# Optimization experiments

Hardware: AMD Instinct MI355X
Metric: run time of the kernel (lower is better)

The kernel has to match this reference:

```python
import jax, jax.numpy as jnp
import numpy as np

N_EMBD = 768
N_HEAD = 12
HEAD_DIM = N_EMBD // N_HEAD
EPS = 1e-6


def setup_inputs() -> dict:
    key = jax.random.key(0)
    ks = jax.random.split(key, 8)
    B, T, C = 4, 2048, N_EMBD
    s = 0.02
    return {
        "x": jax.random.normal(ks[0], (B, T, C), jnp.float32),
        "ln1_w": jnp.ones((C,), jnp.float32),
        "ln1_b": jnp.zeros((C,), jnp.float32),
        "W_attn": jax.random.normal(ks[1], (C, 3 * C), jnp.float32) * s,
        "b_attn": jnp.zeros((3 * C,), jnp.float32),
        "W_attn_proj": jax.random.normal(ks[2], (C, C), jnp.float32) * s,
        "b_attn_proj": jnp.zeros((C,), jnp.float32),
        "ln2_w": jnp.ones((C,), jnp.float32),
        "ln2_b": jnp.zeros((C,), jnp.float32),
        "W_fc": jax.random.normal(ks[3], (C, 4 * C), jnp.float32) * s,
        "b_fc": jnp.zeros((4 * C,), jnp.float32),
        "W_mlp_proj": jax.random.normal(ks[4], (4 * C, C), jnp.float32) * s,
        "b_mlp_proj": jnp.zeros((C,), jnp.float32),
    }


def layer_norm(x, w, b):
    # Faithful to MyLayerNorm: (x - mean) / (std + eps), std with ddof=0
    mean = jnp.mean(x, axis=-1, keepdims=True)
    std = jnp.sqrt(jnp.mean((x - mean) ** 2, axis=-1, keepdims=True))
    return w * (x - mean) / (std + EPS) + b


def attention(h, W_attn, b_attn, W_proj, b_proj):
    B, T, C = h.shape
    qkv = h @ W_attn + b_attn                      # [B,T,3C]
    q, k, v = jnp.split(qkv, 3, axis=-1)
    # [B,T,C] -> [B,H,T,D]
    def to_heads(t):
        return t.reshape(B, T, N_HEAD, HEAD_DIM).transpose(0, 2, 1, 3)
    q, k, v = to_heads(q), to_heads(k), to_heads(v)
    att = jnp.einsum("bhtd,bhsd->bhts", q, k) * (1.0 / np.sqrt(HEAD_DIM))
    causal = jnp.tril(jnp.ones((T, T), bool))[None, None]
    att = jnp.where(causal, att, -jnp.inf)
    att = jax.nn.softmax(att, axis=-1)
    y = jnp.einsum("bhts,bhsd->bhtd", att, v)      # [B,H,T,D]
    y = y.transpose(0, 2, 1, 3).reshape(B, T, C)
    return y @ W_proj + b_proj


def mlp(h, W_fc, b_fc, W_proj, b_proj):
    h = jax.nn.gelu(h @ W_fc + b_fc, approximate=False)
    return h @ W_proj + b_proj


def reference(x, ln1_w, ln1_b, W_attn, b_attn, W_attn_proj, b_attn_proj,
              ln2_w, ln2_b, W_fc, b_fc, W_mlp_proj, b_mlp_proj):
    x = x + attention(layer_norm(x, ln1_w, ln1_b), W_attn, b_attn, W_attn_proj, b_attn_proj)
    x = x + mlp(layer_norm(x, ln2_w, ln2_b), W_fc, b_fc, W_mlp_proj, b_mlp_proj)
    return x
```

## Files before the change

kernel.cpp:

```cpp
#include <hip/hip_runtime.h>
#include <hip/hip_bf16.h>
#include <math.h>

#define N_EMBD 768
#define N_HEAD 12
#define HEAD_DIM 64
#define TOKENS 8192
#define SEQ 2048
#define BATCH 4
#define NQT (SEQ / 64)

typedef __attribute__((ext_vector_type(8))) short short8;
typedef __attribute__((ext_vector_type(4))) float f32x4;

__device__ __forceinline__ short f2bf(float f) {
    unsigned u = __builtin_bit_cast(unsigned, f);
    unsigned r = (u + 0x7fffu + ((u >> 16) & 1u)) >> 16;
    return (short)r;
}
__device__ __forceinline__ short f2bf_fast(float f) {
    unsigned u = __builtin_bit_cast(unsigned, f);
    return (short)((u + 0x8000u) >> 16);
}

__device__ __forceinline__ float gelu_fast(float x) {
    float z = 1.5957691216057308f * x * (1.0f + 0.044715f * x * x);
    return x / (1.0f + __expf(-z));
}

__device__ __forceinline__ void gld16(const void* g, void* l) {
    __builtin_amdgcn_global_load_lds(
        (const __attribute__((address_space(1))) unsigned int*)g,
        (__attribute__((address_space(3))) unsigned int*)l, 16, 0, 0);
}

__global__ __launch_bounds__(256) void wT_kernel(const float* __restrict__ W,
                                                 short* __restrict__ Wt,
                                                 int K, int N) {
    __shared__ float T[32][33];
    int k0 = blockIdx.y * 32, n0 = blockIdx.x * 32;
    int c = threadIdx.x & 31, r0 = threadIdx.x >> 5;
#pragma unroll
    for (int i = 0; i < 32; i += 8)
        T[r0 + i][c] = W[(size_t)(k0 + r0 + i) * N + n0 + c];
    __syncthreads();
#pragma unroll
    for (int i = 0; i < 32; i += 8)
        Wt[(size_t)(n0 + r0 + i) * K + k0 + c] = f2bf(T[c][r0 + i]);
}

__global__ __launch_bounds__(256) void ln_bf_kernel(const float* __restrict__ x,
                                                    const float* __restrict__ w,
                                                    const float* __restrict__ b,
                                                    short* __restrict__ out) {
    int row = blockIdx.x;
    const float* xr = x + (size_t)row * N_EMBD;
    short* yr = out + (size_t)row * N_EMBD;
    __shared__ float red[256];
    int tid = threadIdx.x;
    float v0 = xr[tid], v1 = xr[tid + 256], v2 = xr[tid + 512];
    red[tid] = v0 + v1 + v2; __syncthreads();
    for (int off = 128; off > 0; off >>= 1) {
        if (tid < off) red[tid] += red[tid + off];
        __syncthreads();
    }
    float mean = red[0] * (1.f / 768.f);
    __syncthreads();
    float d0 = v0 - mean, d1 = v1 - mean, d2 = v2 - mean;
    red[tid] = d0 * d0 + d1 * d1 + d2 * d2; __syncthreads();
    for (int off = 128; off > 0; off >>= 1) {
        if (tid < off) red[tid] += red[tid + off];
        __syncthreads();
    }
    float inv = 1.f / (sqrtf(red[0] * (1.f / 768.f)) + 1e-6f);
    yr[tid]       = f2bf(w[tid]       * d0 * inv + b[tid]);
    yr[tid + 256] = f2bf(w[tid + 256] * d1 * inv + b[tid + 256]);
    yr[tid + 512] = f2bf(w[tid + 512] * d2 * inv + b[tid + 512]);
}

template <int ACT, int RES, int OUTBF>
__global__ __launch_bounds__(256) void gemm_mfma(
        const short* __restrict__ A,
        const short* __restrict__ Bt,
        const float* __restrict__ bias,
        const float* __restrict__ res,
        void* __restrict__ outp,
        int M, int N, int K) {
    __shared__ short As[8192];
    __shared__ short Bs[8192];
    int tid = threadIdx.x;
    int wave = tid >> 6, lane = tid & 63;
    int quad = lane >> 4, l15 = lane & 15;
    int m0 = blockIdx.x * 128, n0 = blockIdx.y * 128;
    int wm = wave >> 1, wn = wave & 1;
    int sr = lane >> 2, sc = (lane & 3) * 8;

    f32x4 acc[4][4];
#pragma unroll
    for (int i = 0; i < 4; ++i)
#pragma unroll
        for (int j = 0; j < 4; ++j) acc[i][j] = (f32x4){0.f, 0.f, 0.f, 0.f};

    const short* ag = A + (size_t)(m0 + wave * 32 + sr) * K + sc;
    const short* bg = Bt + (size_t)(n0 + wave * 32 + sr) * K + sc;
    int woff = wave * 1024;

    gld16(ag, &As[woff]);
    gld16(ag + (size_t)16 * K, &As[woff + 512]);
    gld16(bg, &Bs[woff]);
    gld16(bg + (size_t)16 * K, &Bs[woff + 512]);

    int nk = K >> 5;
    for (int it = 0; it < nk; ++it) {
        int cb = (it & 1) * 4096;
        __syncthreads();
        if (it + 1 < nk) {
            int nb = ((it + 1) & 1) * 4096 + woff;
            int kn = (it + 1) << 5;
            gld16(ag + kn, &As[nb]);
            gld16(ag + kn + (size_t)16 * K, &As[nb + 512]);
            gld16(bg + kn, &Bs[nb]);
            gld16(bg + kn + (size_t)16 * K, &Bs[nb + 512]);
        }
        short8 af[4], bfr[4];
#pragma unroll
        for (int mt = 0; mt < 4; ++mt)
            af[mt] = *(const short8*)&As[cb + (wm * 64 + mt * 16 + l15) * 32 + quad * 8];
#pragma unroll
        for (int nt = 0; nt < 4; ++nt)
            bfr[nt] = *(const short8*)&Bs[cb + (wn * 64 + nt * 16 + l15) * 32 + quad * 8];
#pragma unroll
        for (int mt = 0; mt < 4; ++mt)
#pragma unroll
            for (int nt = 0; nt < 4; ++nt)
                acc[mt][nt] = __builtin_amdgcn_mfma_f32_16x16x32_bf16(
                    af[mt], bfr[nt], acc[mt][nt], 0, 0, 0);
    }

#pragma unroll
    for (int mt = 0; mt < 4; ++mt) {
        int row0 = m0 + wm * 64 + mt * 16 + quad * 4;
#pragma unroll
        for (int nt = 0; nt < 4; ++nt) {
            int col = n0 + wn * 64 + nt * 16 + l15;
            float bi = bias[col];
#pragma unroll
            for (int r = 0; r < 4; ++r) {
                float v = acc[mt][nt][r] + bi;
                if (ACT == 1) v = gelu_fast(v);
                if (RES) v += res[(size_t)(row0 + r) * N + col];
                if (OUTBF) ((short*)outp)[(size_t)(row0 + r) * N + col] = f2bf(v);
                else       ((float*)outp)[(size_t)(row0 + r) * N + col] = v;
            }
        }
    }
}

template <int ACT, int RES, int OUTBF>
__global__ __launch_bounds__(256) void gemm_mfma_n64(
        const short* __restrict__ A,
        const short* __restrict__ Bt,
        const float* __restrict__ bias,
        const float* __restrict__ res,
        void* __restrict__ outp,
        int M, int N, int K) {
    __shared__ short As[8192];
    __shared__ short Bs[4096];
    int tid = threadIdx.x;
    int wave = tid >> 6, lane = tid & 63;
    int quad = lane >> 4, l15 = lane & 15;
    int m0 = blockIdx.x * 128, n0 = blockIdx.y * 64;
    int wm = wave >> 1, wn = wave & 1;
    int sr = lane >> 2, sc = (lane & 3) * 8;

    f32x4 acc[4][2];
#pragma unroll
    for (int i = 0; i < 4; ++i)
#pragma unroll
        for (int j = 0; j < 2; ++j) acc[i][j] = (f32x4){0.f, 0.f, 0.f, 0.f};

    const short* gptr[3];
    int loff[3];
    bool isa[3];
#pragma unroll
    for (int j = 0; j < 3; ++j) {
        int c = wave * 3 + j;
        if (c < 8) {
            gptr[j] = A + (size_t)(m0 + c * 16 + sr) * K + sc;
            loff[j] = c * 512; isa[j] = true;
        } else {
            gptr[j] = Bt + (size_t)(n0 + (c - 8) * 16 + sr) * K + sc;
            loff[j] = (c - 8) * 512; isa[j] = false;
        }
    }

#pragma unroll
    for (int j = 0; j < 3; ++j)
        gld16(gptr[j], isa[j] ? &As[loff[j]] : &Bs[loff[j]]);

    int nk = K >> 5;
    for (int it = 0; it < nk; ++it) {
        int cba = (it & 1) * 4096, cbb = (it & 1) * 2048;
        __syncthreads();
        if (it + 1 < nk) {
            int nba = ((it + 1) & 1) * 4096, nbb = ((it + 1) & 1) * 2048;
            int kn = (it + 1) << 5;
#pragma unroll
            for (int j = 0; j < 3; ++j)
                gld16(gptr[j] + kn, isa[j] ? &As[nba + loff[j]] : &Bs[nbb + loff[j]]);
        }
        short8 af[4], bfr[2];
#pragma unroll
        for (int mt = 0; mt < 4; ++mt)
            af[mt] = *(const short8*)&As[cba + (wm * 64 + mt * 16 + l15) * 32 + quad * 8];
#pragma unroll
        for (int nt = 0; nt < 2; ++nt)
            bfr[nt] = *(const short8*)&Bs[cbb + (wn * 32 + nt * 16 + l15) * 32 + quad * 8];
#pragma unroll
        for (int mt = 0; mt < 4; ++mt)
#pragma unroll
            for (int nt = 0; nt < 2; ++nt)
                acc[mt][nt] = __builtin_amdgcn_mfma_f32_16x16x32_bf16(
                    af[mt], bfr[nt], acc[mt][nt], 0, 0, 0);
    }

#pragma unroll
    for (int mt = 0; mt < 4; ++mt) {
        int row0 = m0 + wm * 64 + mt * 16 + quad * 4;
#pragma unroll
        for (int nt = 0; nt < 2; ++nt) {
            int col = n0 + wn * 32 + nt * 16 + l15;
            float bi = bias[col];
#pragma unroll
            for (int r = 0; r < 4; ++r) {
                float v = acc[mt][nt][r] + bi;
                if (ACT == 1) v = gelu_fast(v);
                if (RES) v += res[(size_t)(row0 + r) * N + col];
                if (OUTBF) ((short*)outp)[(size_t)(row0 + r) * N + col] = f2bf(v);
                else       ((float*)outp)[(size_t)(row0 + r) * N + col] = v;
            }
        }
    }
}

__global__ __launch_bounds__(256) void vT_kernel(const short* __restrict__ qkv,
                                                 short* __restrict__ Vt) {
    __shared__ short Ts[64][65];
    int t0 = blockIdx.x * 64;
    int bh = blockIdx.y;
    int h = bh % N_HEAD, b = bh / N_HEAD;
    int tid = threadIdx.x;
    int r = tid >> 3, c8 = (tid & 7) * 8;
    const short* src = qkv + ((size_t)(b * SEQ + t0)) * 2304 + 1536 + h * 64;
#pragma unroll
    for (int p = 0; p < 2; ++p) {
        int rr = r + p * 32;
        short8 v = *(const short8*)(src + (size_t)rr * 2304 + c8);
#pragma unroll
        for (int j = 0; j < 8; ++j) Ts[rr][c8 + j] = v[j];
    }
    __syncthreads();
    int d = tid >> 2, s0 = (tid & 3) * 16;
    short* dst = Vt + ((size_t)bh * 64 + d) * SEQ + t0;
#pragma unroll
    for (int p = 0; p < 2; ++p) {
        int sb = s0 + p * 8;
        short8 v;
#pragma unroll
        for (int j = 0; j < 8; ++j) v[j] = Ts[sb + j][d];
        *(short8*)(dst + sb) = v;
    }
}

__device__ __forceinline__ void attn_tile(
        const short* __restrict__ qkv, const short* __restrict__ Vt,
        short* __restrict__ y, int bh, int qt,
        short* Qs, short* Ks, short* Vs, short* Ps) {
    int tid = threadIdx.x;
    int wave = tid >> 6, lane = tid & 63;
    int quad = lane >> 4, l15 = lane & 15;
    int h = bh % N_HEAD, b = bh / N_HEAD;
    size_t bT = (size_t)b * SEQ;
    int q0 = qt * 64;
    int sr = lane >> 2, sc = (lane & 3) * 8;

    const short ONE_BF = (short)0x3F80;
    short8 ones;
#pragma unroll
    for (int j = 0; j < 8; ++j) ones[j] = ONE_BF;

    __syncthreads();
#pragma unroll
    for (int j = 0; j < 2; ++j) {
        int c = wave * 2 + j;
        int sub = c >> 2, r0 = (c & 3) * 16;
        const short* g = qkv + (bT + q0 + r0 + sr) * 2304 + h * 64 + sub * 32 + sc;
        gld16(g, &Qs[sub * 2048 + r0 * 32]);
    }
    __syncthreads();
    short8 qf[2];
    qf[0] = *(const short8*)&Qs[(wave * 16 + l15) * 32 + quad * 8];
    qf[1] = *(const short8*)&Qs[2048 + (wave * 16 + l15) * 32 + quad * 8];

    f32x4 o[4];
#pragma unroll
    for (int nt = 0; nt < 4; ++nt) o[nt] = (f32x4){0.f, 0.f, 0.f, 0.f};
    f32x4 lacc = (f32x4){0.f, 0.f, 0.f, 0.f};

    for (int kt = 0; kt <= qt; ++kt) {
        int k0 = kt * 64;
        __syncthreads();
#pragma unroll
        for (int j = 0; j < 4; ++j) {
            int c = wave * 4 + j;
            if (c < 8) {
                int sub = c >> 2, r0 = (c & 3) * 16;
                const short* g = qkv + (bT + k0 + r0 + sr) * 2304 + 768 + h * 64 + sub * 32 + sc;
                gld16(g, &Ks[sub * 2048 + r0 * 32]);
            } else {
                int cv = c - 8;
                int sub = cv >> 2, r0 = (cv & 3) * 16;
                const short* g = Vt + ((size_t)bh * 64 + r0 + sr) * SEQ + k0 + sub * 32 + sc;
                gld16(g, &Vs[sub * 2048 + r0 * 32]);
            }
        }
        __syncthreads();

        f32x4 sacc[4];
#pragma unroll
        for (int nt = 0; nt < 4; ++nt) sacc[nt] = (f32x4){0.f, 0.f, 0.f, 0.f};
#pragma unroll
        for (int nt = 0; nt < 4; ++nt)
#pragma unroll
            for (int ks = 0; ks < 2; ++ks) {
                short8 kf = *(const short8*)&Ks[ks * 2048 + (nt * 16 + l15) * 32 + quad * 8];
                sacc[nt] = __builtin_amdgcn_mfma_f32_16x16x32_bf16(qf[ks], kf, sacc[nt], 0, 0, 0);
            }

        bool diag = (kt == qt);
#pragma unroll
        for (int nt = 0; nt < 4; ++nt) {
            int scol = nt * 16 + l15;
            int base = (scol >> 5) * 2048 + (scol & 31);
#pragma unroll
            for (int r = 0; r < 4; ++r) {
                float s = sacc[nt][r] * 0.125f - 4.0f;
                if (diag && (scol > wave * 16 + quad * 4 + r)) s = -1e30f;
                Ps[base + (wave * 16 + quad * 4 + r) * 32] = f2bf_fast(__expf(s));
            }
        }

        short8 pf0 = *(const short8*)&Ps[(wave * 16 + l15) * 32 + quad * 8];
        short8 pf1 = *(const short8*)&Ps[2048 + (wave * 16 + l15) * 32 + quad * 8];
        lacc = __builtin_amdgcn_mfma_f32_16x16x32_bf16(pf0, ones, lacc, 0, 0, 0);
        lacc = __builtin_amdgcn_mfma_f32_16x16x32_bf16(pf1, ones, lacc, 0, 0, 0);
#pragma unroll
        for (int nt = 0; nt < 4; ++nt) {
            short8 vf0 = *(const short8*)&Vs[(nt * 16 + l15) * 32 + quad * 8];
            short8 vf1 = *(const short8*)&Vs[2048 + (nt * 16 + l15) * 32 + quad * 8];
            o[nt] = __builtin_amdgcn_mfma_f32_16x16x32_bf16(pf0, vf0, o[nt], 0, 0, 0);
            o[nt] = __builtin_amdgcn_mfma_f32_16x16x32_bf16(pf1, vf1, o[nt], 0, 0, 0);
        }
    }

    float inv[4];
#pragma unroll
    for (int r = 0; r < 4; ++r) inv[r] = 1.f / lacc[r];
#pragma unroll
    for (int nt = 0; nt < 4; ++nt)
#pragma unroll
        for (int r = 0; r < 4; ++r)
            y[(bT + q0 + wave * 16 + quad * 4 + r) * N_EMBD + h * 64 + nt * 16 + l15] =
                f2bf(o[nt][r] * inv[r]);
}

__global__ __launch_bounds__(256) void attn_mfma(
        const short* __restrict__ qkv, const short* __restrict__ Vt,
        short* __restrict__ y) {
    __shared__ short Qs[4096], Ks[4096], Vs[4096], Ps[4096];
    int bh = blockIdx.x;
    int pair = blockIdx.y;
    attn_tile(qkv, Vt, y, bh, pair, Qs, Ks, Vs, Ps);
    attn_tile(qkv, Vt, y, bh, NQT - 1 - pair, Qs, Ks, Vs, Ps);
}

extern "C" void kernel_launch(void* const* d_in, const int* in_sizes, int n_in,
                              void* d_out, int out_size, void* d_ws, size_t ws_size,
                              hipStream_t stream) {
    const float* x         = (const float*)d_in[0];
    const float* ln1_w     = (const float*)d_in[1];
    const float* ln1_b     = (const float*)d_in[2];
    const float* W_attn    = (const float*)d_in[3];
    const float* b_attn    = (const float*)d_in[4];
    const float* W_attn_pr = (const float*)d_in[5];
    const float* b_attn_pr = (const float*)d_in[6];
    const float* ln2_w     = (const float*)d_in[7];
    const float* ln2_b     = (const float*)d_in[8];
    const float* W_fc      = (const float*)d_in[9];
    const float* b_fc      = (const float*)d_in[10];
    const float* W_mlp_pr  = (const float*)d_in[11];
    const float* b_mlp_pr  = (const float*)d_in[12];
    float* out = (float*)d_out;

    const int M = TOKENS, C = N_EMBD;
    char* ws = (char*)d_ws;
    size_t region0 = (size_t)M * 3072 * 2;
    short* qkv_bf = (short*)ws;
    short* fc_bf  = (short*)ws;
    size_t off = region0;
    short* VtB   = (short*)(ws + off); off += (size_t)48 * 64 * SEQ * 2;
    short* yb    = (short*)(ws + off); off += (size_t)M * C * 2;
    short* lnb   = (short*)(ws + off); off += (size_t)M * C * 2;
    float* x1    = (float*)(ws + off); off += (size_t)M * C * 4;
    short* WaT   = (short*)(ws + off); off += (size_t)2304 * 768 * 2;
    short* WpT   = (short*)(ws + off); off += (size_t)768 * 768 * 2;
    short* WfT   = (short*)(ws + off); off += (size_t)3072 * 768 * 2;
    short* WmT   = (short*)(ws + off); off += (size_t)768 * 3072 * 2;

    wT_kernel<<<dim3(2304 / 32, 768 / 32), 256, 0, stream>>>(W_attn, WaT, 768, 2304);
    wT_kernel<<<dim3(768 / 32, 768 / 32), 256, 0, stream>>>(W_attn_pr, WpT, 768, 768);
    wT_kernel<<<dim3(3072 / 32, 768 / 32), 256, 0, stream>>>(W_fc, WfT, 768, 3072);
    wT_kernel<<<dim3(768 / 32, 3072 / 32), 256, 0, stream>>>(W_mlp_pr, WmT, 3072, 768);

    ln_bf_kernel<<<M, 256, 0, stream>>>(x, ln1_w, ln1_b, lnb);

    gemm_mfma<0, 0, 1><<<dim3(M / 128, 2304 / 128), 256, 0, stream>>>(
        lnb, WaT, b_attn, nullptr, qkv_bf, M, 2304, 768);

    vT_kernel<<<dim3(SEQ / 64, BATCH * N_HEAD), 256, 0, stream>>>(qkv_bf, VtB);

    attn_mfma<<<dim3(BATCH * N_HEAD, NQT / 2), 256, 0, stream>>>(qkv_bf, VtB, yb);

    gemm_mfma_n64<0, 1, 0><<<dim3(M / 128, 768 / 64), 256, 0, stream>>>(
        yb, WpT, b_attn_pr, x, x1, M, 768, 768);

    ln_bf_kernel<<<M, 256, 0, stream>>>(x1, ln2_w, ln2_b, lnb);

    gemm_mfma<1, 0, 1><<<dim3(M / 128, 3072 / 128), 256, 0, stream>>>(
        lnb, WfT, b_fc, nullptr, fc_bf, M, 3072, 768);

    gemm_mfma_n64<0, 1, 0><<<dim3(M / 128, 768 / 64), 256, 0, stream>>>(
        fc_bf, WmT, b_mlp_pr, x1, out, M, 768, 3072);
}
```

Before: 379.0 us.

## Fuse V transpose into QKV GEMM, double-buffer attention K/V, merge weight transposes

Four changes land together. The QKV GEMM writes its V columns straight into the transposed Vt layout, which removes the separate vT kernel and its extra read and write of V. Attention double-buffers the K/V tiles in LDS so the next tile's loads overlap the current tile's MFMAs, dropping one barrier per iteration at the cost of twice the K/V shared memory. The four weight-transpose launches become a single kernel, and layernorm moves to one wave per row with float4 loads and shuffle reductions instead of a block-wide LDS tree.

```diff
diff --git a/kernel.cpp b/kernel.cpp
--- a/kernel.cpp
+++ b/kernel.cpp
@@ -11,6 +11,7 @@
 #define NQT (SEQ / 64)
 
 typedef __attribute__((ext_vector_type(8))) short short8;
+typedef __attribute__((ext_vector_type(4))) short short4v;
 typedef __attribute__((ext_vector_type(4))) float f32x4;
 
 __device__ __forceinline__ short f2bf(float f) {
@@ -34,11 +35,20 @@
         (__attribute__((address_space(3))) unsigned int*)l, 16, 0, 0);
 }
 
-__global__ __launch_bounds__(256) void wT_kernel(const float* __restrict__ W,
-                                                 short* __restrict__ Wt,
-                                                 int K, int N) {
+__global__ __launch_bounds__(256) void wT_all(
+        const float* __restrict__ Wa, short* __restrict__ Ta,
+        const float* __restrict__ Wp, short* __restrict__ Tp,
+        const float* __restrict__ Wf, short* __restrict__ Tf,
+        const float* __restrict__ Wm, short* __restrict__ Tm) {
     __shared__ float T[32][33];
-    int k0 = blockIdx.y * 32, n0 = blockIdx.x * 32;
+    int id = blockIdx.x;
+    const float* W; short* Wt; int K, N;
+    if (id < 1728)      { W = Wa; Wt = Ta; K = 768;  N = 2304; }
+    else if (id < 2304) { W = Wp; Wt = Tp; K = 768;  N = 768;  id -= 1728; }
+    else if (id < 4608) { W = Wf; Wt = Tf; K = 768;  N = 3072; id -= 2304; }
+    else                { W = Wm; Wt = Tm; K = 3072; N = 768;  id -= 4608; }
+    int tn = N >> 5;
+    int n0 = (id % tn) * 32, k0 = (id / tn) * 32;
     int c = threadIdx.x & 31, r0 = threadIdx.x >> 5;
 #pragma unroll
     for (int i = 0; i < 32; i += 8)
@@ -53,38 +63,54 @@
                                                     const float* __restrict__ w,
                                                     const float* __restrict__ b,
                                                     short* __restrict__ out) {
-    int row = blockIdx.x;
-    const float* xr = x + (size_t)row * N_EMBD;
-    short* yr = out + (size_t)row * N_EMBD;
-    __shared__ float red[256];
-    int tid = threadIdx.x;
-    float v0 = xr[tid], v1 = xr[tid + 256], v2 = xr[tid + 512];
-    red[tid] = v0 + v1 + v2; __syncthreads();
-    for (int off = 128; off > 0; off >>= 1) {
-        if (tid < off) red[tid] += red[tid + off];
-        __syncthreads();
-    }
-    float mean = red[0] * (1.f / 768.f);
-    __syncthreads();
-    float d0 = v0 - mean, d1 = v1 - mean, d2 = v2 - mean;
-    red[tid] = d0 * d0 + d1 * d1 + d2 * d2; __syncthreads();
-    for (int off = 128; off > 0; off >>= 1) {
-        if (tid < off) red[tid] += red[tid + off];
-        __syncthreads();
-    }
-    float inv = 1.f / (sqrtf(red[0] * (1.f / 768.f)) + 1e-6f);
-    yr[tid]       = f2bf(w[tid]       * d0 * inv + b[tid]);
-    yr[tid + 256] = f2bf(w[tid + 256] * d1 * inv + b[tid + 256]);
-    yr[tid + 512] = f2bf(w[tid + 512] * d2 * inv + b[tid + 512]);
-}
-
-template <int ACT, int RES, int OUTBF>
+    int row = blockIdx.x * 4 + (threadIdx.x >> 6);
+    int lane = threadIdx.x & 63;
+    const float4* xr = (const float4*)(x + (size_t)row * N_EMBD);
+    const float4* wr = (const float4*)w;
+    const float4* br = (const float4*)b;
+
+    float4 v[3];
+#pragma unroll
+    for (int i = 0; i < 3; ++i) v[i] = xr[lane + 64 * i];
+    float s = 0.f;
+#pragma unroll
+    for (int i = 0; i < 3; ++i) s += v[i].x + v[i].y + v[i].z + v[i].w;
+#pragma unroll
+    for (int off = 1; off < 64; off <<= 1) s += __shfl_xor(s, off, 64);
+    float mean = s * (1.f / 768.f);
+
+    float var = 0.f;
+#pragma unroll
+    for (int i = 0; i < 3; ++i) {
+        float a0 = v[i].x - mean, a1 = v[i].y - mean,
+              a2 = v[i].z - mean, a3 = v[i].w - mean;
+        var += a0 * a0 + a1 * a1 + a2 * a2 + a3 * a3;
+    }
+#pragma unroll
+    for (int off = 1; off < 64; off <<= 1) var += __shfl_xor(var, off, 64);
+    float inv = 1.f / (sqrtf(var * (1.f / 768.f)) + 1e-6f);
+
+    short4v* yr = (short4v*)(out + (size_t)row * N_EMBD);
+#pragma unroll
+    for (int i = 0; i < 3; ++i) {
+        float4 wv = wr[lane + 64 * i], bv = br[lane + 64 * i];
+        short4v o;
+        o[0] = f2bf(wv.x * (v[i].x - mean) * inv + bv.x);
+        o[1] = f2bf(wv.y * (v[i].y - mean) * inv + bv.y);
+        o[2] = f2bf(wv.z * (v[i].z - mean) * inv + bv.z);
+        o[3] = f2bf(wv.w * (v[i].w - mean) * inv + bv.w);
+        yr[lane + 64 * i] = o;
+    }
+}
+
+template <int ACT, int RES, int OUTBF, int VOUT>
 __global__ __launch_bounds__(256) void gemm_mfma(
         const short* __restrict__ A,
         const short* __restrict__ Bt,
         const float* __restrict__ bias,
         const float* __restrict__ res,
         void* __restrict__ outp,
+        short* __restrict__ vt,
         int M, int N, int K) {
     __shared__ short As[8192];
     __shared__ short Bs[8192];
@@ -135,6 +161,27 @@
             for (int nt = 0; nt < 4; ++nt)
                 acc[mt][nt] = __builtin_amdgcn_mfma_f32_16x16x32_bf16(
                     af[mt], bfr[nt], acc[mt][nt], 0, 0, 0);
+    }
+
+    if (VOUT && n0 >= 1536) {
+#pragma unroll
+        for (int mt = 0; mt < 4; ++mt) {
+            int row0 = m0 + wm * 64 + mt * 16 + quad * 4;
+            int b = row0 >> 11, t0 = row0 & 2047;
+#pragma unroll
+            for (int nt = 0; nt < 4; ++nt) {
+                int col = n0 + wn * 64 + nt * 16 + l15;
+                int vcol = col - 1536;
+                int bh = b * N_HEAD + (vcol >> 6);
+                int d = vcol & 63;
+                float bi = bias[col];
+                short4v o;
+#pragma unroll
+                for (int r = 0; r < 4; ++r) o[r] = f2bf(acc[mt][nt][r] + bi);
+                *(short4v*)&vt[((size_t)bh * 64 + d) * SEQ + t0] = o;
+            }
+        }
+        return;
     }
 
 #pragma unroll
@@ -243,35 +290,6 @@
     }
 }
 
-__global__ __launch_bounds__(256) void vT_kernel(const short* __restrict__ qkv,
-                                                 short* __restrict__ Vt) {
-    __shared__ short Ts[64][65];
-    int t0 = blockIdx.x * 64;
-    int bh = blockIdx.y;
-    int h = bh % N_HEAD, b = bh / N_HEAD;
-    int tid = threadIdx.x;
-    int r = tid >> 3, c8 = (tid & 7) * 8;
-    const short* src = qkv + ((size_t)(b * SEQ + t0)) * 2304 + 1536 + h * 64;
-#pragma unroll
-    for (int p = 0; p < 2; ++p) {
-        int rr = r + p * 32;
-        short8 v = *(const short8*)(src + (size_t)rr * 2304 + c8);
-#pragma unroll
-        for (int j = 0; j < 8; ++j) Ts[rr][c8 + j] = v[j];
-    }
-    __syncthreads();
-    int d = tid >> 2, s0 = (tid & 3) * 16;
-    short* dst = Vt + ((size_t)bh * 64 + d) * SEQ + t0;
-#pragma unroll
-    for (int p = 0; p < 2; ++p) {
-        int sb = s0 + p * 8;
-        short8 v;
-#pragma unroll
-        for (int j = 0; j < 8; ++j) v[j] = Ts[sb + j][d];
-        *(short8*)(dst + sb) = v;
-    }
-}
-
 __device__ __forceinline__ void attn_tile(
         const short* __restrict__ qkv, const short* __restrict__ Vt,
         short* __restrict__ y, int bh, int qt,
@@ -297,6 +315,20 @@
         const short* g = qkv + (bT + q0 + r0 + sr) * 2304 + h * 64 + sub * 32 + sc;
         gld16(g, &Qs[sub * 2048 + r0 * 32]);
     }
+#pragma unroll
+    for (int j = 0; j < 4; ++j) {
+        int c = wave * 4 + j;
+        if (c < 8) {
+            int sub = c >> 2, r0 = (c & 3) * 16;
+            const short* g = qkv + (bT + r0 + sr) * 2304 + 768 + h * 64 + sub * 32 + sc;
+            gld16(g, &Ks[sub * 2048 + r0 * 32]);
+        } else {
+            int cv = c - 8;
+            int sub = cv >> 2, r0 = (cv & 3) * 16;
+            const short* g = Vt + ((size_t)bh * 64 + r0 + sr) * SEQ + sub * 32 + sc;
+            gld16(g, &Vs[sub * 2048 + r0 * 32]);
+        }
+    }
     __syncthreads();
     short8 qf[2];
     qf[0] = *(const short8*)&Qs[(wave * 16 + l15) * 32 + quad * 8];
@@ -308,23 +340,26 @@
     f32x4 lacc = (f32x4){0.f, 0.f, 0.f, 0.f};
 
     for (int kt = 0; kt <= qt; ++kt) {
-        int k0 = kt * 64;
-        __syncthreads();
-#pragma unroll
-        for (int j = 0; j < 4; ++j) {
-            int c = wave * 4 + j;
-            if (c < 8) {
-                int sub = c >> 2, r0 = (c & 3) * 16;
-                const short* g = qkv + (bT + k0 + r0 + sr) * 2304 + 768 + h * 64 + sub * 32 + sc;
-                gld16(g, &Ks[sub * 2048 + r0 * 32]);
-            } else {
-                int cv = c - 8;
-                int sub = cv >> 2, r0 = (cv & 3) * 16;
-                const short* g = Vt + ((size_t)bh * 64 + r0 + sr) * SEQ + k0 + sub * 32 + sc;
-                gld16(g, &Vs[sub * 2048 + r0 * 32]);
-            }
-        }
-        __syncthreads();
+        int cb = (kt & 1) * 4096;
+        if (kt) __syncthreads();
+        if (kt < qt) {
+            int nb = ((kt + 1) & 1) * 4096;
+            int k0n = (kt + 1) * 64;
+#pragma unroll
+            for (int j = 0; j < 4; ++j) {
+                int c = wave * 4 + j;
+                if (c < 8) {
+                    int sub = c >> 2, r0 = (c & 3) * 16;
+                    const short* g = qkv + (bT + k0n + r0 + sr) * 2304 + 768 + h * 64 + sub * 32 + sc;
+                    gld16(g, &Ks[nb + sub * 2048 + r0 * 32]);
+                } else {
+                    int cv = c - 8;
+                    int sub = cv >> 2, r0 = (cv & 3) * 16;
+                    const short* g = Vt + ((size_t)bh * 64 + r0 + sr) * SEQ + k0n + sub * 32 + sc;
+                    gld16(g, &Vs[nb + sub * 2048 + r0 * 32]);
+                }
+            }
+        }
 
         f32x4 sacc[4];
 #pragma unroll
@@ -333,7 +368,7 @@
         for (int nt = 0; nt < 4; ++nt)
 #pragma unroll
             for (int ks = 0; ks < 2; ++ks) {
-                short8 kf = *(const short8*)&Ks[ks * 2048 + (nt * 16 + l15) * 32 + quad * 8];
+                short8 kf = *(const short8*)&Ks[cb + ks * 2048 + (nt * 16 + l15) * 32 + quad * 8];
                 sacc[nt] = __builtin_amdgcn_mfma_f32_16x16x32_bf16(qf[ks], kf, sacc[nt], 0, 0, 0);
             }
 
@@ -356,8 +391,8 @@
         lacc = __builtin_amdgcn_mfma_f32_16x16x32_bf16(pf1, ones, lacc, 0, 0, 0);
 #pragma unroll
         for (int nt = 0; nt < 4; ++nt) {
-            short8 vf0 = *(const short8*)&Vs[(nt * 16 + l15) * 32 + quad * 8];
-            short8 vf1 = *(const short8*)&Vs[2048 + (nt * 16 + l15) * 32 + quad * 8];
+            short8 vf0 = *(const short8*)&Vs[cb + (nt * 16 + l15) * 32 + quad * 8];
+            short8 vf1 = *(const short8*)&Vs[cb + 2048 + (nt * 16 + l15) * 32 + quad * 8];
             o[nt] = __builtin_amdgcn_mfma_f32_16x16x32_bf16(pf0, vf0, o[nt], 0, 0, 0);
             o[nt] = __builtin_amdgcn_mfma_f32_16x16x32_bf16(pf1, vf1, o[nt], 0, 0, 0);
         }
@@ -377,7 +412,7 @@
 __global__ __launch_bounds__(256) void attn_mfma(
         const short* __restrict__ qkv, const short* __restrict__ Vt,
         short* __restrict__ y) {
-    __shared__ short Qs[4096], Ks[4096], Vs[4096], Ps[4096];
+    __shared__ short Qs[4096], Ks[8192], Vs[8192], Ps[4096];
     int bh = blockIdx.x;
     int pair = blockIdx.y;
     attn_tile(qkv, Vt, y, bh, pair, Qs, Ks, Vs, Ps);
@@ -417,27 +452,23 @@
     short* WfT   = (short*)(ws + off); off += (size_t)3072 * 768 * 2;
     short* WmT   = (short*)(ws + off); off += (size_t)768 * 3072 * 2;
 
-    wT_kernel<<<dim3(2304 / 32, 768 / 32), 256, 0, stream>>>(W_attn, WaT, 768, 2304);
-    wT_kernel<<<dim3(768 / 32, 768 / 32), 256, 0, stream>>>(W_attn_pr, WpT, 768, 768);
-    wT_kernel<<<dim3(3072 / 32, 768 / 32), 256, 0, stream>>>(W_fc, WfT, 768, 3072);
-    wT_kernel<<<dim3(768 / 32, 3072 / 32), 256, 0, stream>>>(W_mlp_pr, WmT, 3072, 768);
-
-    ln_bf_kernel<<<M, 256, 0, stream>>>(x, ln1_w, ln1_b, lnb);
-
-    gemm_mfma<0, 0, 1><<<dim3(M / 128, 2304 / 128), 256, 0, stream>>>(
-        lnb, WaT, b_attn, nullptr, qkv_bf, M, 2304, 768);
-
-    vT_kernel<<<dim3(SEQ / 64, BATCH * N_HEAD), 256, 0, stream>>>(qkv_bf, VtB);
+    wT_all<<<6912, 256, 0, stream>>>(W_attn, WaT, W_attn_pr, WpT,
+                                     W_fc, WfT, W_mlp_pr, WmT);
+
+    ln_bf_kernel<<<M / 4, 256, 0, stream>>>(x, ln1_w, ln1_b, lnb);
+
+    gemm_mfma<0, 0, 1, 1><<<dim3(M / 128, 2304 / 128), 256, 0, stream>>>(
+        lnb, WaT, b_attn, nullptr, qkv_bf, VtB, M, 2304, 768);
 
     attn_mfma<<<dim3(BATCH * N_HEAD, NQT / 2), 256, 0, stream>>>(qkv_bf, VtB, yb);
 
     gemm_mfma_n64<0, 1, 0><<<dim3(M / 128, 768 / 64), 256, 0, stream>>>(
         yb, WpT, b_attn_pr, x, x1, M, 768, 768);
 
-    ln_bf_kernel<<<M, 256, 0, stream>>>(x1, ln2_w, ln2_b, lnb);
-
-    gemm_mfma<1, 0, 1><<<dim3(M / 128, 3072 / 128), 256, 0, stream>>>(
-        lnb, WfT, b_fc, nullptr, fc_bf, M, 3072, 768);
+    ln_bf_kernel<<<M / 4, 256, 0, stream>>>(x1, ln2_w, ln2_b, lnb);
+
+    gemm_mfma<1, 0, 1, 0><<<dim3(M / 128, 3072 / 128), 256, 0, stream>>>(
+        lnb, WfT, b_fc, nullptr, fc_bf, nullptr, M, 3072, 768);
 
     gemm_mfma_n64<0, 1, 0><<<dim3(M / 128, 768 / 64), 256, 0, stream>>>(
         fc_bf, WmT, b_mlp_pr, x1, out, M, 768, 3072);
```

Measured after the change: 376.0 us. Within noise of the previous version (-0.8%).
